# Kernel tuning notes

Hardware: AMD Instinct MI355X
Metric: run time of the kernel (lower is better)

The kernel has to match this reference:

```python
import jax, jax.numpy as jnp
import numpy as np

STATE_DIM = 128
HIDDEN = 128
NUM_HEADS = 16
TEMPERATURE = 1.0
NEG_INF = float('-inf')


def setup_inputs() -> dict:
    key = jax.random.key(0)
    ks = jax.random.split(key, 8)
    B, S = 2, 512
    state_embeddings = jax.random.normal(ks[0], (B, S, STATE_DIM), dtype=jnp.float32)
    mask = jnp.ones((B, S, S), dtype=bool)
    # MLP params (Linear stores [in, out] here; we apply x @ W + b)
    W1 = jax.random.normal(ks[1], (2 * STATE_DIM, HIDDEN), dtype=jnp.float32) / np.sqrt(2 * STATE_DIM)
    b1 = jnp.zeros((HIDDEN,), dtype=jnp.float32)
    W2 = jax.random.normal(ks[2], (HIDDEN, HIDDEN), dtype=jnp.float32) / np.sqrt(HIDDEN)
    b2 = jnp.zeros((HIDDEN,), dtype=jnp.float32)
    W3 = jax.random.normal(ks[3], (HIDDEN, NUM_HEADS), dtype=jnp.float32) / np.sqrt(HIDDEN)
    b3 = jnp.zeros((NUM_HEADS,), dtype=jnp.float32)
    head_temperatures = jnp.ones((NUM_HEADS,), dtype=jnp.float32) * TEMPERATURE
    return {
        'state_embeddings': state_embeddings,
        'mask': mask,
        'W1': W1, 'b1': b1, 'W2': W2, 'b2': b2, 'W3': W3, 'b3': b3,
        'head_temperatures': head_temperatures,
    }


def reference(state_embeddings, mask, W1, b1, W2, b2, W3, b3, head_temperatures):
    # Split first Linear: cat([x_i, x_j]) @ W1 == x_i @ W1a + x_j @ W1b
    # This avoids materializing the [B, S, S, 2*state_dim] pairwise concat
    # while computing identical math.
    W1a, W1b = W1[:STATE_DIM], W1[STATE_DIM:]
    hi = jnp.einsum('bsd,dh->bsh', state_embeddings, W1a) + b1  # [B,S,H]
    hj = jnp.einsum('bsd,dh->bsh', state_embeddings, W1b)       # [B,S,H]
    h = jax.nn.relu(hi[:, :, None, :] + hj[:, None, :, :])       # [B,S,S,H]
    h = jax.nn.relu(jnp.einsum('bijh,hk->bijk', h, W2) + b2)     # [B,S,S,H]
    comp = jnp.einsum('bijh,hn->bijn', h, W3) + b3               # [B,S,S,heads]
    bias = jnp.transpose(comp, (0, 3, 1, 2))                     # [B,heads,S,S]
    bias = bias * head_temperatures[None, :, None, None]
    bias = jnp.where(mask[:, None, :, :], bias, NEG_INF)
    return bias
```

## Files before the change

### kernel.cpp

```cpp
#include <hip/hip_runtime.h>
#include <math.h>

typedef _Float16 half8 __attribute__((ext_vector_type(8)));
typedef _Float16 half4v __attribute__((ext_vector_type(4)));
typedef float floatx4 __attribute__((ext_vector_type(4)));

__global__ __launch_bounds__(256) void prep_kernel(
    const float* __restrict__ E,
    const float* __restrict__ W1,
    const float* __restrict__ b1,
    const float* __restrict__ W2,
    const float* __restrict__ W3,
    _Float16* __restrict__ hih,
    _Float16* __restrict__ hjF,
    _Float16* __restrict__ W2frag,
    _Float16* __restrict__ W3frag)
{
    const int blk = blockIdx.x;
    const int t = threadIdx.x;
    if (blk < 1024) {
        __shared__ float sE[128];
        if (t < 128) sE[t] = E[blk*128 + t];
        __syncthreads();
        const int half = t >> 7;
        const int k = t & 127;
        float acc = half ? 0.f : b1[k];
        const float* w1col = &W1[half*128*128 + k];
        #pragma unroll 8
        for (int d = 0; d < 128; ++d)
            acc = fmaf(sE[d], w1col[d*128], acc);
        if (half == 0) {
            hih[blk*128 + k] = (_Float16)acc;
        } else {
            const int jt = blk >> 4, lr = blk & 15;
            const int ks = k >> 5, lq = (k >> 3) & 3, q = k & 7;
            hjF[(((jt*4 + ks)*64) + lq*16 + lr)*8 + q] = (_Float16)acc;
        }
    } else if (blk == 1024) {
        for (int e = t; e < 16384; e += 256) {
            int q = e & 7, l = (e >> 3) & 63, g = e >> 9;
            int wr = g >> 4, nt = (g >> 2) & 3, ks = g & 3;
            int row = 64*wr + 16*nt + (l & 15);
            int k = ks*32 + (l >> 4)*8 + q;
            W2frag[e] = (_Float16)W2[k*128 + row];
        }
    } else {
        for (int e = t; e < 2048; e += 256) {
            int q = e & 7, l = (e >> 3) & 63, ks = e >> 9;
            int k = ks*32 + (l >> 4)*8 + q;
            W3frag[e] = (_Float16)W3[k*16 + (l & 15)];
        }
    }
}

__global__ __launch_bounds__(256, 3) void main_kernel(
    const _Float16* __restrict__ hih,
    const _Float16* __restrict__ hjF,
    const _Float16* __restrict__ W2frag,
    const _Float16* __restrict__ W3frag,
    const float* __restrict__ b2,
    const float* __restrict__ b3,
    const float* __restrict__ temps,
    const int* __restrict__ mask,
    float* __restrict__ out)
{
    constexpr int PADH = 136;
    __shared__ _Float16 sH[128 * PADH];

    const int tid = threadIdx.x;
    const int bid = blockIdx.x;
    const int b  = bid >> 11;
    const int i  = (bid >> 2) & 511;
    const int j0 = (bid & 3) << 7;

    const int lane = tid & 63;
    const int wave = tid >> 6;
    const int wr = wave >> 1;
    const int wc = wave & 1;
    const int lr = lane & 15;
    const int lq = lane >> 4;

    const half8 zero8 = {};
    const _Float16* hirow = &hih[(b*512 + i)*128];
    const half8* w2v = (const half8*)W2frag;
    const half8* w3v = (const half8*)W3frag;
    const half8* hjv = (const half8*)hjF;
    const int jt0 = b*32 + (bid & 3)*8 + wc*4;

    half8 aW[4][4];
    #pragma unroll
    for (int nt = 0; nt < 4; ++nt)
        #pragma unroll
        for (int ks = 0; ks < 4; ++ks)
            aW[nt][ks] = w2v[((wr*4 + nt)*4 + ks)*64 + lane];

    half8 hiF[4];
    #pragma unroll
    for (int ks = 0; ks < 4; ++ks)
        hiF[ks] = *(const half8*)&hirow[ks*32 + lq*8];
    const int* mrow = &mask[(b*512 + i)*512];
    const int m0e = 32*wave;
    const int4 mk0 = *(const int4*)&mrow[j0 + m0e + 4*lq];
    const int4 mk1 = *(const int4*)&mrow[j0 + m0e + 16 + 4*lq];

    floatx4 acc[4][4] = {};
    #pragma unroll
    for (int ks = 0; ks < 4; ++ks) {
        half8 bF[4];
        #pragma unroll
        for (int mt = 0; mt < 4; ++mt) {
            half8 hj8 = hjv[((jt0 + mt)*4 + ks)*64 + lane];
            bF[mt] = __builtin_elementwise_max(hiF[ks] + hj8, zero8);
        }
        #pragma unroll
        for (int nt = 0; nt < 4; ++nt)
            #pragma unroll
            for (int mt = 0; mt < 4; ++mt)
                acc[nt][mt] = __builtin_amdgcn_mfma_f32_16x16x32_f16(
                    aW[nt][ks], bF[mt], acc[nt][mt], 0, 0, 0);
    }

    #pragma unroll
    for (int nt = 0; nt < 4; ++nt) {
        const int nb = 64*wr + 16*nt + 4*lq;
        const float4 bv = *(const float4*)&b2[nb];
        #pragma unroll
        for (int mt = 0; mt < 4; ++mt) {
            const int m = 64*wc + 16*mt + lr;
            floatx4 v = acc[nt][mt];
            half4v o;
            o[0] = (_Float16)fmaxf(v[0] + bv.x, 0.f);
            o[1] = (_Float16)fmaxf(v[1] + bv.y, 0.f);
            o[2] = (_Float16)fmaxf(v[2] + bv.z, 0.f);
            o[3] = (_Float16)fmaxf(v[3] + bv.w, 0.f);
            *(half4v*)&sH[m*PADH + nb] = o;
        }
    }
    __syncthreads();

    floatx4 acc2[2] = {};
    #pragma unroll
    for (int ks = 0; ks < 4; ++ks) {
        const int k0 = ks*32 + lq*8;
        half8 bW = w3v[ks*64 + lane];
        half8 a0 = *(const half8*)&sH[(m0e + lr)*PADH + k0];
        half8 a1 = *(const half8*)&sH[(m0e + 16 + lr)*PADH + k0];
        acc2[0] = __builtin_amdgcn_mfma_f32_16x16x32_f16(a0, bW, acc2[0], 0, 0, 0);
        acc2[1] = __builtin_amdgcn_mfma_f32_16x16x32_f16(a1, bW, acc2[1], 0, 0, 0);
    }

    const int n2 = lr;
    const float tempv = temps[n2];
    const float b3v = b3[n2];
    float* outp = &out[(((b*16 + n2)*512) + i)*512];
    {
        const int j = j0 + m0e + 4*lq;
        floatx4 v = acc2[0];
        float4 res;
        res.x = mk0.x ? (v[0] + b3v)*tempv : -INFINITY;
        res.y = mk0.y ? (v[1] + b3v)*tempv : -INFINITY;
        res.z = mk0.z ? (v[2] + b3v)*tempv : -INFINITY;
        res.w = mk0.w ? (v[3] + b3v)*tempv : -INFINITY;
        *(float4*)&outp[j] = res;
    }
    {
        const int j = j0 + m0e + 16 + 4*lq;
        floatx4 v = acc2[1];
        float4 res;
        res.x = mk1.x ? (v[0] + b3v)*tempv : -INFINITY;
        res.y = mk1.y ? (v[1] + b3v)*tempv : -INFINITY;
        res.z = mk1.z ? (v[2] + b3v)*tempv : -INFINITY;
        res.w = mk1.w ? (v[3] + b3v)*tempv : -INFINITY;
        *(float4*)&outp[j] = res;
    }
}

extern "C" void kernel_launch(void* const* d_in, const int* in_sizes, int n_in,
                              void* d_out, int out_size, void* d_ws, size_t ws_size,
                              hipStream_t stream)
{
    const float* E     = (const float*)d_in[0];
    const int* mask    = (const int*)d_in[1];
    const float* W1    = (const float*)d_in[2];
    const float* b1    = (const float*)d_in[3];
    const float* W2    = (const float*)d_in[4];
    const float* b2    = (const float*)d_in[5];
    const float* W3    = (const float*)d_in[6];
    const float* b3    = (const float*)d_in[7];
    const float* temps = (const float*)d_in[8];

    char* ws = (char*)d_ws;
    _Float16* hih = (_Float16*)ws;
    _Float16* hjF = (_Float16*)(ws + 262144);
    _Float16* W2f = (_Float16*)(ws + 524288);
    _Float16* W3f = W2f + 16384;

    prep_kernel<<<1026, 256, 0, stream>>>(E, W1, b1, W2, W3, hih, hjF, W2f, W3f);
    main_kernel<<<4096, 256, 0, stream>>>(hih, hjF, W2f, W3f, b2, b3, temps, mask,
                                          (float*)d_out);
}
```

Before: 120.4 us.

## Stage hj tile in LDS via direct global-to-LDS loads, reuse buffer in fragment layout

Each block now copies its 128-column hj tile into shared memory once using global_load_lds, and waves read their B operands from LDS instead of each fetching them from global memory. The same 32KB buffer is then reused for the layer-2 activations, stored in MFMA fragment order rather than as padded rows. This shrinks LDS per block so the occupancy hint can go from 3 to 4 blocks. It adds two extra barriers and risks LDS bank conflicts with the unpadded fragment layout.

```diff
diff --git a/kernel.cpp b/kernel.cpp
--- a/kernel.cpp
+++ b/kernel.cpp
@@ -53,7 +53,7 @@
     }
 }
 
-__global__ __launch_bounds__(256, 3) void main_kernel(
+__global__ __launch_bounds__(256, 4) void main_kernel(
     const _Float16* __restrict__ hih,
     const _Float16* __restrict__ hjF,
     const _Float16* __restrict__ W2frag,
@@ -64,8 +64,7 @@
     const int* __restrict__ mask,
     float* __restrict__ out)
 {
-    constexpr int PADH = 136;
-    __shared__ _Float16 sH[128 * PADH];
+    __shared__ _Float16 sB[16384];
 
     const int tid = threadIdx.x;
     const int bid = blockIdx.x;
@@ -80,12 +79,25 @@
     const int lr = lane & 15;
     const int lq = lane >> 4;
 
+    const _Float16* gsrc = hjF + (size_t)((b*32 + (bid & 3)*8)*4) * 512;
+    #pragma unroll
+    for (int f8 = 0; f8 < 8; ++f8) {
+        const int f = wave*8 + f8;
+        const _Float16* src = gsrc + f*512 + lane*8;
+        _Float16* dst = &sB[f*512];
+#if __has_builtin(__builtin_amdgcn_global_load_lds)
+        __builtin_amdgcn_global_load_lds(
+            (const __attribute__((address_space(1))) void*)src,
+            (__attribute__((address_space(3))) void*)dst, 16, 0, 0);
+#else
+        *(half8*)(dst + lane*8) = *(const half8*)src;
+#endif
+    }
+
     const half8 zero8 = {};
     const _Float16* hirow = &hih[(b*512 + i)*128];
     const half8* w2v = (const half8*)W2frag;
     const half8* w3v = (const half8*)W3frag;
-    const half8* hjv = (const half8*)hjF;
-    const int jt0 = b*32 + (bid & 3)*8 + wc*4;
 
     half8 aW[4][4];
     #pragma unroll
@@ -98,18 +110,21 @@
     #pragma unroll
     for (int ks = 0; ks < 4; ++ks)
         hiF[ks] = *(const half8*)&hirow[ks*32 + lq*8];
+
     const int* mrow = &mask[(b*512 + i)*512];
     const int m0e = 32*wave;
     const int4 mk0 = *(const int4*)&mrow[j0 + m0e + 4*lq];
     const int4 mk1 = *(const int4*)&mrow[j0 + m0e + 16 + 4*lq];
 
+    __syncthreads();
+
     floatx4 acc[4][4] = {};
     #pragma unroll
     for (int ks = 0; ks < 4; ++ks) {
         half8 bF[4];
         #pragma unroll
         for (int mt = 0; mt < 4; ++mt) {
-            half8 hj8 = hjv[((jt0 + mt)*4 + ks)*64 + lane];
+            half8 hj8 = *(const half8*)&sB[((4*wc + mt)*4 + ks)*512 + lane*8];
             bF[mt] = __builtin_elementwise_max(hiF[ks] + hj8, zero8);
         }
         #pragma unroll
@@ -119,21 +134,24 @@
                 acc[nt][mt] = __builtin_amdgcn_mfma_f32_16x16x32_f16(
                     aW[nt][ks], bF[mt], acc[nt][mt], 0, 0, 0);
     }
+    __syncthreads();
 
     #pragma unroll
     for (int nt = 0; nt < 4; ++nt) {
         const int nb = 64*wr + 16*nt + 4*lq;
         const float4 bv = *(const float4*)&b2[nb];
+        const int ks2 = 2*wr + (nt >> 1);
+        const int l2 = lr + 16*(2*(nt & 1) + (lq >> 1));
         #pragma unroll
         for (int mt = 0; mt < 4; ++mt) {
-            const int m = 64*wc + 16*mt + lr;
+            const int frag = (2*wc + (mt >> 1))*8 + (mt & 1)*4 + ks2;
             floatx4 v = acc[nt][mt];
             half4v o;
             o[0] = (_Float16)fmaxf(v[0] + bv.x, 0.f);
             o[1] = (_Float16)fmaxf(v[1] + bv.y, 0.f);
             o[2] = (_Float16)fmaxf(v[2] + bv.z, 0.f);
             o[3] = (_Float16)fmaxf(v[3] + bv.w, 0.f);
-            *(half4v*)&sH[m*PADH + nb] = o;
+            *(half4v*)&sB[frag*512 + l2*8 + 4*(lq & 1)] = o;
         }
     }
     __syncthreads();
@@ -141,10 +159,9 @@
     floatx4 acc2[2] = {};
     #pragma unroll
     for (int ks = 0; ks < 4; ++ks) {
-        const int k0 = ks*32 + lq*8;
         half8 bW = w3v[ks*64 + lane];
-        half8 a0 = *(const half8*)&sH[(m0e + lr)*PADH + k0];
-        half8 a1 = *(const half8*)&sH[(m0e + 16 + lr)*PADH + k0];
+        half8 a0 = *(const half8*)&sB[(wave*8 + ks)*512 + lane*8];
+        half8 a1 = *(const half8*)&sB[(wave*8 + 4 + ks)*512 + lane*8];
         acc2[0] = __builtin_amdgcn_mfma_f32_16x16x32_f16(a0, bW, acc2[0], 0, 0, 0);
         acc2[1] = __builtin_amdgcn_mfma_f32_16x16x32_f16(a1, bW, acc2[1], 0, 0, 0);
     }
```

Result: slower. 154.7 us (+28.5%).
